# Kernel tuning notes

Hardware: AMD Instinct MI355X
Metric: run time of the kernel (lower is better)

## Reference

```python
import jax, jax.numpy as jnp
import numpy as np

GRID_SIZE = 16
KH = KW = 3


def setup_inputs() -> dict:
    key = jax.random.key(0)
    k1, k2, k3, k4 = jax.random.split(key, 4)
    B, H, W, C, F = 8, 32, 32, 64, 64
    x = jax.random.normal(k1, (B, H, W, C), dtype=jnp.float32)
    control_points = jax.random.normal(k2, (F, C, KH, KW, GRID_SIZE), dtype=jnp.float32) * 0.1
    w1 = jax.random.normal(k3, (F, C, KH, KW), dtype=jnp.float32) * 0.1
    w2 = jax.random.normal(k4, (F, C, KH, KW), dtype=jnp.float32) * 0.1
    return {"x": x, "control_points": control_points, "w1": w1, "w2": w2}


def _extract_patches_same(x, kh, kw):
    # x: (B,H,W,C), stride 1, TF 'SAME' padding -> (B,H,W,kh,kw,C)
    B, H, W, C = x.shape
    ph, pw = kh - 1, kw - 1
    xp = jnp.pad(x, ((0, 0), (ph // 2, ph - ph // 2), (pw // 2, pw - pw // 2), (0, 0)))
    taps = [xp[:, i:i + H, j:j + W, :] for i in range(kh) for j in range(kw)]
    return jnp.stack(taps, axis=3).reshape(B, H, W, kh, kw, C)


def reference(x, control_points, w1, w2):
    F, C, kh, kw, G = control_points.shape
    grid = jnp.linspace(-1.0, 1.0, G)
    patches = _extract_patches_same(x, kh, kw)  # (B,H,W,kh,kw,C)
    # spline: searchsorted + clip + linear interp on the fixed uniform grid
    xc = jnp.clip(patches, -1.0, 1.0)
    idx = jnp.clip(jnp.searchsorted(grid, xc, side='left') - 1, 0, G - 2)
    frac = (xc - grid[idx]) / (grid[idx + 1] - grid[idx])  # (B,H,W,kh,kw,C)
    # two-nonzero linear basis over control points -> (B,H,W,kh,kw,C,G)
    basis = (jax.nn.one_hot(idx, G, dtype=x.dtype) * (1.0 - frac)[..., None]
             + jax.nn.one_hot(idx + 1, G, dtype=x.dtype) * frac[..., None])
    # fuse w1 into control points, contract taps+channels+grid in one einsum
    wcp = w1[..., None] * control_points  # (F,C,kh,kw,G)
    out = jnp.einsum('bpqijcg,fcijg->bpqf', basis, wcp)
    out = out + jnp.einsum('bpqijc,fcij->bpqf', jax.nn.silu(patches), w2)
    return out  # (B,H,W,F)
```

## Files before the change

kernel.cpp:

```cpp
#include <hip/hip_runtime.h>


typedef _Float16 v8h __attribute__((ext_vector_type(8)));
typedef float    v4f __attribute__((ext_vector_type(4)));

#define NSLOT8  81920
#define NOUT4   131072

__global__ __launch_bounds__(256) void prep_wsw(const float* __restrict__ cp,
                                                const float* __restrict__ w1,
                                                const float* __restrict__ w2,
                                                _Float16* __restrict__ wsw,
                                                float* __restrict__ out) {
    int tid = blockIdx.x * 256 + threadIdx.x;
    if (tid < NSLOT8) {
        int lane = tid & 63;
        int rest = tid >> 6;
        int nt   = rest & 3;
        int ks   = rest >> 2;
        int kb   = ks * 32 + ((lane >> 4) << 3);
        int f    = (nt << 4) + (lane & 15);
        int chunk = kb / 640;
        int klb   = kb - chunk * 640;
        v8h o;
        if (klb < 576) {
            int c  = (chunk << 2) + klb / 144;
            int rb = klb % 144;
            int ij = rb >> 4;
            float w = w1[f * 576 + c * 9 + ij];
            const v4f* cpp = (const v4f*)(cp + (size_t)f * 9216 + c * 144 + rb);
            v4f lo = cpp[0], hi = cpp[1];
#pragma unroll
            for (int j = 0; j < 4; ++j) {
                o[j]     = (_Float16)(w * lo[j]);
                o[j + 4] = (_Float16)(w * hi[j]);
            }
        } else {
            int i2 = klb - 576;
            int c  = (chunk << 2) + (i2 >> 4);
            if ((i2 & 15) == 0) {
#pragma unroll
                for (int j = 0; j < 8; ++j)
                    o[j] = (_Float16)w2[f * 576 + c * 9 + j];
            } else {
#pragma unroll
                for (int j = 0; j < 8; ++j) o[j] = (_Float16)0.f;
                o[0] = (_Float16)w2[f * 576 + c * 9 + 8];
            }
        }
        ((v8h*)wsw)[tid] = o;
    }
    if (tid < NOUT4) ((v4f*)out)[tid] = (v4f){0.f, 0.f, 0.f, 0.f};
}

__global__ __launch_bounds__(512, 8) void kan_mfma(const float* __restrict__ x,
                                                   const _Float16* __restrict__ wsw,
                                                   float* __restrict__ out) {
    __shared__ __align__(16) char smem[40960];
    float* red = (float*)smem;

    int blk   = blockIdx.x;
    int kh    = blk >> 8;
    int rowid = blk & 255;
    int b = rowid >> 5, p = rowid & 31;
    int t = threadIdx.x, wv = t >> 6, lane = t & 63;
    int m = lane & 15, kq = lane >> 4;
    int wg = wv >> 1, nh = wv & 1;

    int ch0 = kh * 4, ch1 = ch0 + 4;
    const float* xb = x + (size_t)b * 65536;

    bool act = t < 288;
    int xoff, sbase, smask, ijb;
    {
        int e  = act ? t : 0;
        int q  = e / 9;
        int ij = e - q * 9;
        int di = ij / 3;
        int dj = ij - di * 3;
        int row = p + di - 1;
        int col = q + dj - 1;
        bool ok = ((unsigned)row < 32u) && ((unsigned)col < 32u) && act;
        xoff  = ok ? (row * 32 + col) * 64 : -1;
        sbase = q * 1280;
        smask = (q & 7) << 4;
        ijb   = ij * 32;
    }

    v4f z4 = (v4f){0.f, 0.f, 0.f, 0.f};
    v4f acc[2][2];
#pragma unroll
    for (int i = 0; i < 2; ++i)
#pragma unroll
        for (int n = 0; n < 2; ++n) acc[i][n] = z4;

    for (int i4 = t; i4 < 2560; i4 += 512) ((v4f*)smem)[i4] = z4;

    v4f vbuf = (xoff >= 0) ? *(const v4f*)(xb + xoff + ch0 * 4) : z4;
    unsigned pk = 0u;

    __syncthreads();

    for (int gch = ch0; gch < ch1; ++gch) {
        if (act) {
            v4f xv = vbuf;
            char* rowp = smem + sbase;
            unsigned pp = pk, np = 0;
#pragma unroll
            for (int cl = 0; cl < 4; ++cl) {
                float v  = xv[cl];
                float xc = fminf(fmaxf(v, -1.f), 1.f);
                float tt = (xc + 1.f) * 7.5f;
                int idx  = (int)tt;
                if (idx > 14) idx = 14;
                float fr = tt - (float)idx;
                float sv = v * __builtin_amdgcn_rcpf(1.f + __expf(-v));
                int sb0 = cl * 288 + ijb;
                if (gch > ch0) {
                    int pb = sb0 + (int)((pp >> (cl * 8)) & 255) * 2;
                    *(_Float16*)(rowp + (pb ^ smask))       = (_Float16)0.f;
                    *(_Float16*)(rowp + ((pb + 2) ^ smask)) = (_Float16)0.f;
                }
                int wb = sb0 + idx * 2;
                *(_Float16*)(rowp + (wb ^ smask))       = (_Float16)(1.f - fr);
                *(_Float16*)(rowp + ((wb + 2) ^ smask)) = (_Float16)fr;
                *(_Float16*)(rowp + ((1152 + cl * 32 + (ijb >> 4)) ^ smask))
                    = (_Float16)sv;
                np |= (unsigned)idx << (cl * 8);
            }
            pk = np;
        }
        __syncthreads();
        if (gch + 1 < ch1)
            vbuf = (xoff >= 0) ? *(const v4f*)(xb + xoff + (gch + 1) * 4) : z4;
        const v8h* bp = (const v8h*)wsw
                      + ((size_t)gch * 20 + wg * 5) * 256 + nh * 128 + lane;
        int mbase = m * 1280;
        int mm    = (m & 7) << 4;
#pragma unroll
        for (int s = 0; s < 5; ++s) {
            int kx = (((wg * 5 + s) * 64) + (kq * 16)) ^ mm;
            v8h a0 = *(const v8h*)(smem + mbase + kx);
            v8h a1 = *(const v8h*)(smem + mbase + 20480 + kx);
            v8h b0 = bp[s * 256];
            v8h b1 = bp[s * 256 + 64];
            acc[0][0] = __builtin_amdgcn_mfma_f32_16x16x32_f16(a0, b0, acc[0][0], 0, 0, 0);
            acc[0][1] = __builtin_amdgcn_mfma_f32_16x16x32_f16(a0, b1, acc[0][1], 0, 0, 0);
            acc[1][0] = __builtin_amdgcn_mfma_f32_16x16x32_f16(a1, b0, acc[1][0], 0, 0, 0);
            acc[1][1] = __builtin_amdgcn_mfma_f32_16x16x32_f16(a1, b1, acc[1][1], 0, 0, 0);
        }
        __syncthreads();
    }

#pragma unroll
    for (int mt = 0; mt < 2; ++mt)
#pragma unroll
        for (int ntl = 0; ntl < 2; ++ntl)
#pragma unroll
            for (int r = 0; r < 4; ++r)
                red[wg * 2080 + (mt * 16 + kq * 4 + r) * 65
                    + (nh * 2 + ntl) * 16 + m] = acc[mt][ntl][r];
    __syncthreads();
    int f = t & 63, pg = t >> 6;
    float* op = out + (size_t)rowid * 2048 + f;
#pragma unroll
    for (int i = 0; i < 4; ++i) {
        int px = pg * 4 + i;
        float s = red[px * 65 + f] + red[2080 + px * 65 + f]
                + red[4160 + px * 65 + f] + red[6240 + px * 65 + f];
        atomicAdd(op + px * 64, s);
    }
}

extern "C" void kernel_launch(void* const* d_in, const int* in_sizes, int n_in,
                              void* d_out, int out_size, void* d_ws, size_t ws_size,
                              hipStream_t stream) {
    const float* x  = (const float*)d_in[0];
    const float* cp = (const float*)d_in[1];
    const float* w1 = (const float*)d_in[2];
    const float* w2 = (const float*)d_in[3];
    _Float16* wsw = (_Float16*)d_ws;
    float*    outp = (float*)d_out;

    prep_wsw<<<512, 256, 0, stream>>>(cp, w1, w2, wsw, outp);
    kan_mfma<<<1024, 512, 0, stream>>>(x, wsw, outp);
}
```

Baseline: 82.18 us.

## Double-buffer spline basis in LDS to overlap scatter with MFMA

Adds a second LDS buffer so the basis/silu scatter for the next channel group is written while MFMAs consume the current one, which removes one barrier per iteration. B-operand global loads are software-prefetched one step ahead, and s_setprio is raised around the MFMA loop. LDS use doubles to 80KB and the occupancy hint drops from 8 to 4 blocks, which may reduce latency hiding.

```diff
diff --git a/kernel.cpp b/kernel.cpp
--- a/kernel.cpp
+++ b/kernel.cpp
@@ -6,6 +6,7 @@
 
 #define NSLOT8  81920
 #define NOUT4   131072
+#define BUFB    40960
 
 __global__ __launch_bounds__(256) void prep_wsw(const float* __restrict__ cp,
                                                 const float* __restrict__ w1,
@@ -53,10 +54,40 @@
     if (tid < NOUT4) ((v4f*)out)[tid] = (v4f){0.f, 0.f, 0.f, 0.f};
 }
 
-__global__ __launch_bounds__(512, 8) void kan_mfma(const float* __restrict__ x,
+__device__ __forceinline__ void scatter4(v4f xv, char* __restrict__ base,
+                                         int sbase, int smask, int ijb,
+                                         unsigned& pk, bool doClear) {
+    char* rowp = base + sbase;
+    unsigned pp = pk, np = 0;
+#pragma unroll
+    for (int cl = 0; cl < 4; ++cl) {
+        float v  = xv[cl];
+        float xc = fminf(fmaxf(v, -1.f), 1.f);
+        float tt = (xc + 1.f) * 7.5f;
+        int idx  = (int)tt;
+        if (idx > 14) idx = 14;
+        float fr = tt - (float)idx;
+        float sv = v * __builtin_amdgcn_rcpf(1.f + __expf(-v));
+        int sb0 = cl * 288 + ijb;
+        if (doClear) {
+            int pb = sb0 + (int)((pp >> (cl * 8)) & 255) * 2;
+            *(_Float16*)(rowp + (pb ^ smask))       = (_Float16)0.f;
+            *(_Float16*)(rowp + ((pb + 2) ^ smask)) = (_Float16)0.f;
+        }
+        int wb = sb0 + idx * 2;
+        *(_Float16*)(rowp + (wb ^ smask))       = (_Float16)(1.f - fr);
+        *(_Float16*)(rowp + ((wb + 2) ^ smask)) = (_Float16)fr;
+        *(_Float16*)(rowp + ((1152 + cl * 32 + (ijb >> 4)) ^ smask))
+            = (_Float16)sv;
+        np |= (unsigned)idx << (cl * 8);
+    }
+    pk = np;
+}
+
+__global__ __launch_bounds__(512, 4) void kan_mfma(const float* __restrict__ x,
                                                    const _Float16* __restrict__ wsw,
                                                    float* __restrict__ out) {
-    __shared__ __align__(16) char smem[40960];
+    __shared__ __align__(16) char smem[2 * BUFB];
     float* red = (float*)smem;
 
     int blk   = blockIdx.x;
@@ -67,7 +98,7 @@
     int m = lane & 15, kq = lane >> 4;
     int wg = wv >> 1, nh = wv & 1;
 
-    int ch0 = kh * 4, ch1 = ch0 + 4;
+    int ch0 = kh * 4;
     const float* xb = x + (size_t)b * 65536;
 
     bool act = t < 288;
@@ -94,61 +125,51 @@
 #pragma unroll
         for (int n = 0; n < 2; ++n) acc[i][n] = z4;
 
-    for (int i4 = t; i4 < 2560; i4 += 512) ((v4f*)smem)[i4] = z4;
+    for (int i4 = t; i4 < 5120; i4 += 512) ((v4f*)smem)[i4] = z4;
 
     v4f vbuf = (xoff >= 0) ? *(const v4f*)(xb + xoff + ch0 * 4) : z4;
-    unsigned pk = 0u;
+    unsigned pkA = 0u, pkB = 0u;
 
     __syncthreads();
 
-    for (int gch = ch0; gch < ch1; ++gch) {
-        if (act) {
-            v4f xv = vbuf;
-            char* rowp = smem + sbase;
-            unsigned pp = pk, np = 0;
-#pragma unroll
-            for (int cl = 0; cl < 4; ++cl) {
-                float v  = xv[cl];
-                float xc = fminf(fmaxf(v, -1.f), 1.f);
-                float tt = (xc + 1.f) * 7.5f;
-                int idx  = (int)tt;
-                if (idx > 14) idx = 14;
-                float fr = tt - (float)idx;
-                float sv = v * __builtin_amdgcn_rcpf(1.f + __expf(-v));
-                int sb0 = cl * 288 + ijb;
-                if (gch > ch0) {
-                    int pb = sb0 + (int)((pp >> (cl * 8)) & 255) * 2;
-                    *(_Float16*)(rowp + (pb ^ smask))       = (_Float16)0.f;
-                    *(_Float16*)(rowp + ((pb + 2) ^ smask)) = (_Float16)0.f;
-                }
-                int wb = sb0 + idx * 2;
-                *(_Float16*)(rowp + (wb ^ smask))       = (_Float16)(1.f - fr);
-                *(_Float16*)(rowp + ((wb + 2) ^ smask)) = (_Float16)fr;
-                *(_Float16*)(rowp + ((1152 + cl * 32 + (ijb >> 4)) ^ smask))
-                    = (_Float16)sv;
-                np |= (unsigned)idx << (cl * 8);
-            }
-            pk = np;
-        }
-        __syncthreads();
-        if (gch + 1 < ch1)
-            vbuf = (xoff >= 0) ? *(const v4f*)(xb + xoff + (gch + 1) * 4) : z4;
+    if (act) scatter4(vbuf, smem, sbase, smask, ijb, pkA, false);
+    vbuf = (xoff >= 0) ? *(const v4f*)(xb + xoff + (ch0 + 1) * 4) : z4;
+    __syncthreads();
+
+    int mbase = m * 1280;
+    int mm    = (m & 7) << 4;
+
+#pragma unroll
+    for (int gi = 0; gi < 4; ++gi) {
+        int g = ch0 + gi;
+        if (gi < 3 && act) {
+            if ((gi & 1) == 0)
+                scatter4(vbuf, smem + BUFB, sbase, smask, ijb, pkB, gi >= 1);
+            else
+                scatter4(vbuf, smem, sbase, smask, ijb, pkA, gi >= 1);
+        }
+        if (gi < 2)
+            vbuf = (xoff >= 0) ? *(const v4f*)(xb + xoff + (g + 2) * 4) : z4;
+
+        char* abuf = smem + (gi & 1) * BUFB;
         const v8h* bp = (const v8h*)wsw
-                      + ((size_t)gch * 20 + wg * 5) * 256 + nh * 128 + lane;
-        int mbase = m * 1280;
-        int mm    = (m & 7) << 4;
+                      + ((size_t)g * 20 + wg * 5) * 256 + nh * 128 + lane;
+        v8h b0c = bp[0], b1c = bp[64];
+        __builtin_amdgcn_s_setprio(1);
 #pragma unroll
         for (int s = 0; s < 5; ++s) {
+            v8h b0n, b1n;
+            if (s < 4) { b0n = bp[(s + 1) * 256]; b1n = bp[(s + 1) * 256 + 64]; }
             int kx = (((wg * 5 + s) * 64) + (kq * 16)) ^ mm;
-            v8h a0 = *(const v8h*)(smem + mbase + kx);
-            v8h a1 = *(const v8h*)(smem + mbase + 20480 + kx);
-            v8h b0 = bp[s * 256];
-            v8h b1 = bp[s * 256 + 64];
-            acc[0][0] = __builtin_amdgcn_mfma_f32_16x16x32_f16(a0, b0, acc[0][0], 0, 0, 0);
-            acc[0][1] = __builtin_amdgcn_mfma_f32_16x16x32_f16(a0, b1, acc[0][1], 0, 0, 0);
-            acc[1][0] = __builtin_amdgcn_mfma_f32_16x16x32_f16(a1, b0, acc[1][0], 0, 0, 0);
-            acc[1][1] = __builtin_amdgcn_mfma_f32_16x16x32_f16(a1, b1, acc[1][1], 0, 0, 0);
-        }
+            v8h a0 = *(const v8h*)(abuf + mbase + kx);
+            v8h a1 = *(const v8h*)(abuf + mbase + 20480 + kx);
+            acc[0][0] = __builtin_amdgcn_mfma_f32_16x16x32_f16(a0, b0c, acc[0][0], 0, 0, 0);
+            acc[0][1] = __builtin_amdgcn_mfma_f32_16x16x32_f16(a0, b1c, acc[0][1], 0, 0, 0);
+            acc[1][0] = __builtin_amdgcn_mfma_f32_16x16x32_f16(a1, b0c, acc[1][0], 0, 0, 0);
+            acc[1][1] = __builtin_amdgcn_mfma_f32_16x16x32_f16(a1, b1c, acc[1][1], 0, 0, 0);
+            if (s < 4) { b0c = b0n; b1c = b1n; }
+        }
+        __builtin_amdgcn_s_setprio(0);
         __syncthreads();
     }
 
```

After: 87.23 us. 1.06x slower.
